# Optimization experiments

Hardware: AMD Instinct MI355X
Metric: run time of the kernel (lower is better)

The kernel has to match this reference:

```python
import jax, jax.numpy as jnp
import numpy as np

THRESH = 0.7
MIN_KEPT = 100000
IGNORE_LABEL = -100.0
LOG_CLAMP = -100.0  # torch binary_cross_entropy clamps log terms at -100

SHAPE = (32, 1, 1024, 1024)

def setup_inputs() -> dict:
    key = jax.random.key(0)
    k1, k2, k3 = jax.random.split(key, 3)
    eps = 1e-6
    predict = jax.random.uniform(k1, SHAPE, dtype=jnp.float32, minval=eps, maxval=1.0 - eps)
    target = jax.random.uniform(k2, SHAPE, dtype=jnp.float32)
    weight = jax.random.uniform(k3, SHAPE, dtype=jnp.float32)
    return {"predict": predict, "target": target, "weight": weight}

def reference(predict, target, weight):
    p = predict.reshape(-1)
    t = target.reshape(-1)
    w = weight.reshape(-1)

    mask = t != IGNORE_LABEL            # valid pixels
    n_valid = jnp.sum(mask)

    # k-th smallest valid probability -> OHEM threshold
    # (push ignored entries to +inf so they sort to the end)
    sort_p = jnp.sort(jnp.where(mask, p, jnp.inf))
    k = jnp.minimum(MIN_KEPT, n_valid - 1)
    min_threshold = sort_p[k]
    threshold = jnp.maximum(min_threshold, THRESH)

    # weighted BCE per element (torch semantics: clamp log at -100)
    logp = jnp.clip(jnp.log(p), LOG_CLAMP)
    log1mp = jnp.clip(jnp.log1p(-p), LOG_CLAMP)
    loss = -w * (t * logp + (1.0 - t) * log1mp)

    # selecting sorted losses where sort_prob < threshold == selecting
    # valid elements with p < threshold (sorting is a permutation)
    sel = mask & (p < threshold)
    total = jnp.sum(jnp.where(sel, loss, 0.0))
    count = jnp.sum(sel).astype(loss.dtype)
    return total / count  # reduction='elementwise_mean'
```

## Files before the change

kernel.cpp:

```cpp
#include <hip/hip_runtime.h>


#define OHEM_THRESH 0.7f
#define OHEM_MIN_KEPT 100000ULL
#define OHEM_IGNORE -100.0f
#define OHEM_LOG_CLAMP -100.0f

#define OHEM_BLOCKS 2048
#define OHEM_TPB 256

__device__ __forceinline__ void ohem_elem(float pp, float tt, float ww,
                                          float& lsum, unsigned int& lcnt,
                                          unsigned int& lval) {
    bool valid = (tt != OHEM_IGNORE);
    bool sel = valid && (pp < OHEM_THRESH);
    float logp = fmaxf(__logf(pp), OHEM_LOG_CLAMP);
    float log1mp = fmaxf(__logf(1.0f - pp), OHEM_LOG_CLAMP);
    float loss = -ww * (tt * logp + (1.0f - tt) * log1mp);
    lval += valid ? 1u : 0u;
    if (sel) {
        lsum += loss;
        lcnt += 1u;
    }
}

__global__ __launch_bounds__(OHEM_TPB, 4) void ohem_reduce(
    const float4* __restrict__ p4, const float4* __restrict__ t4,
    const float4* __restrict__ w4, float* __restrict__ psum,
    unsigned int* __restrict__ pcnt, unsigned int* __restrict__ pval,
    size_t n4, int NB, size_t G) {
    const int tid = threadIdx.x;
    const size_t g = (size_t)blockIdx.x * OHEM_TPB + tid;

    float lsum0 = 0.0f, lsum1 = 0.0f;
    unsigned int lcnt = 0, lval = 0;

    float4 pa0, pa1, ta0, ta1, wa0, wa1;
    float4 pb0, pb1, tb0, tb1, wb0, wb1;

#define LOADA(k)                                        \
    {                                                   \
        size_t i0 = (size_t)(k) * 2 * G + g;            \
        pa0 = p4[i0]; pa1 = p4[i0 + G];                 \
        ta0 = t4[i0]; ta1 = t4[i0 + G];                 \
        wa0 = w4[i0]; wa1 = w4[i0 + G];                 \
    }
#define LOADB(k)                                        \
    {                                                   \
        size_t i0 = (size_t)(k) * 2 * G + g;            \
        pb0 = p4[i0]; pb1 = p4[i0 + G];                 \
        tb0 = t4[i0]; tb1 = t4[i0 + G];                 \
        wb0 = w4[i0]; wb1 = w4[i0 + G];                 \
    }
#define COMP4(pv, tv, wv, ls)                           \
    {                                                   \
        ohem_elem(pv.x, tv.x, wv.x, ls, lcnt, lval);    \
        ohem_elem(pv.y, tv.y, wv.y, ls, lcnt, lval);    \
        ohem_elem(pv.z, tv.z, wv.z, ls, lcnt, lval);    \
        ohem_elem(pv.w, tv.w, wv.w, ls, lcnt, lval);    \
    }

    if (NB > 0) {
        LOADA(0);
        int k = 0;
        while (k + 2 <= NB) {
            LOADB(k + 1);
            __builtin_amdgcn_sched_barrier(0);
            COMP4(pa0, ta0, wa0, lsum0);
            COMP4(pa1, ta1, wa1, lsum1);
            if (k + 2 < NB) LOADA(k + 2);
            __builtin_amdgcn_sched_barrier(0);
            COMP4(pb0, tb0, wb0, lsum0);
            COMP4(pb1, tb1, wb1, lsum1);
            k += 2;
        }
        if (k < NB) {
            COMP4(pa0, ta0, wa0, lsum0);
            COMP4(pa1, ta1, wa1, lsum1);
        }
    }
    for (size_t i = (size_t)NB * 2 * G + g; i < n4; i += G) {
        float4 pv = p4[i];
        float4 tv = t4[i];
        float4 wv = w4[i];
        COMP4(pv, tv, wv, lsum0);
    }

    float lsum = lsum0 + lsum1;
#pragma unroll
    for (int off = 32; off > 0; off >>= 1) {
        lsum += __shfl_down(lsum, off, 64);
        lcnt += __shfl_down(lcnt, off, 64);
        lval += __shfl_down(lval, off, 64);
    }
    __shared__ float s_sum[4];
    __shared__ unsigned int s_cnt[4], s_val[4];
    const int wave = tid >> 6, lane = tid & 63;
    if (lane == 0) {
        s_sum[wave] = lsum;
        s_cnt[wave] = lcnt;
        s_val[wave] = lval;
    }
    __syncthreads();
    if (tid == 0) {
        psum[blockIdx.x] = s_sum[0] + s_sum[1] + s_sum[2] + s_sum[3];
        pcnt[blockIdx.x] = s_cnt[0] + s_cnt[1] + s_cnt[2] + s_cnt[3];
        pval[blockIdx.x] = s_val[0] + s_val[1] + s_val[2] + s_val[3];
    }
}

__global__ __launch_bounds__(256) void ohem_finalize(
    const float* __restrict__ p, const float* __restrict__ t,
    const float* __restrict__ w, const float* __restrict__ psum,
    const unsigned int* __restrict__ pcnt,
    const unsigned int* __restrict__ pval, int nblocks, int tail_start, int n,
    float* __restrict__ out) {
    const int tid = threadIdx.x;
    double dsum = 0.0;
    unsigned long long cnt = 0, val = 0;
    for (int i = tid; i < nblocks; i += 256) {
        dsum += (double)psum[i];
        cnt += pcnt[i];
        val += pval[i];
    }
    for (int i = tail_start + tid; i < n; i += 256) {
        float lsum = 0.0f;
        unsigned int lcnt = 0, lval = 0;
        ohem_elem(p[i], t[i], w[i], lsum, lcnt, lval);
        dsum += (double)lsum;
        cnt += lcnt;
        val += lval;
    }
#pragma unroll
    for (int off = 32; off > 0; off >>= 1) {
        dsum += __shfl_down(dsum, off, 64);
        cnt += __shfl_down(cnt, off, 64);
        val += __shfl_down(val, off, 64);
    }
    __shared__ double s_sum[4];
    __shared__ unsigned long long s_cnt[4], s_val[4];
    const int wave = tid >> 6, lane = tid & 63;
    if (lane == 0) {
        s_sum[wave] = dsum;
        s_cnt[wave] = cnt;
        s_val[wave] = val;
    }
    __syncthreads();
    if (tid == 0) {
        double fsum = s_sum[0] + s_sum[1] + s_sum[2] + s_sum[3];
        unsigned long long fcnt = s_cnt[0] + s_cnt[1] + s_cnt[2] + s_cnt[3];
        unsigned long long fval = s_val[0] + s_val[1] + s_val[2] + s_val[3];
        if (fval == 0) {
            out[0] = __builtin_nanf("");
            return;
        }
        unsigned long long k =
            (OHEM_MIN_KEPT < fval - 1) ? OHEM_MIN_KEPT : fval - 1;
        out[0] = (fcnt > k) ? (float)(fsum / (double)fcnt) : __builtin_nanf("");
    }
}

extern "C" void kernel_launch(void* const* d_in, const int* in_sizes, int n_in,
                              void* d_out, int out_size, void* d_ws,
                              size_t ws_size, hipStream_t stream) {
    const float* predict = (const float*)d_in[0];
    const float* target = (const float*)d_in[1];
    const float* weight = (const float*)d_in[2];
    float* out = (float*)d_out;
    const int n = in_sizes[0];
    const size_t n4 = (size_t)(n >> 2);
    const size_t G = (size_t)OHEM_BLOCKS * OHEM_TPB;
    const int NB = (int)(n4 / (2 * G));

    float* psum = (float*)d_ws;
    unsigned int* pcnt = (unsigned int*)(psum + OHEM_BLOCKS);
    unsigned int* pval = pcnt + OHEM_BLOCKS;

    hipLaunchKernelGGL(ohem_reduce, dim3(OHEM_BLOCKS), dim3(OHEM_TPB), 0,
                       stream, (const float4*)predict, (const float4*)target,
                       (const float4*)weight, psum, pcnt, pval, n4, NB, G);
    hipLaunchKernelGGL(ohem_finalize, dim3(1), dim3(256), 0, stream, predict,
                       target, weight, psum, pcnt, pval, OHEM_BLOCKS,
                       (int)(n4 << 2), n, out);
}
```

Before: 357.7 us.

## Replace double-buffered loads with 4-slot rotating inline-asm load pipeline

Replaces the two-stage A/B double buffer with a four-deep rotating pipeline built from inline-asm global_load_dwordx4 and explicit s_waitcnt vmcnt counters. Each slot is consumed and immediately refilled, so about nine loads stay in flight per thread while one group is computed. The goal is more memory-level parallelism on a bandwidth-bound streaming reduction. In exchange it raises register pressure, and the hand-written waitcnt accounting is fragile against compiler-inserted memory ops.

```diff
diff --git a/kernel.cpp b/kernel.cpp
--- a/kernel.cpp
+++ b/kernel.cpp
@@ -8,6 +8,9 @@
 
 #define OHEM_BLOCKS 2048
 #define OHEM_TPB 256
+#define OHEM_D 4
+
+typedef float f32x4 __attribute__((ext_vector_type(4)));
 
 __device__ __forceinline__ void ohem_elem(float pp, float tt, float ww,
                                           float& lsum, unsigned int& lcnt,
@@ -24,65 +27,78 @@
     }
 }
 
+#define COMP4(pv, tv, wv, ls)                                 \
+    {                                                         \
+        ohem_elem(pv[0], tv[0], wv[0], ls, lcnt, lval);       \
+        ohem_elem(pv[1], tv[1], wv[1], ls, lcnt, lval);       \
+        ohem_elem(pv[2], tv[2], wv[2], ls, lcnt, lval);       \
+        ohem_elem(pv[3], tv[3], wv[3], ls, lcnt, lval);       \
+    }
+
+#define GLOADX4(dst, ptr)                                                  \
+    asm volatile("global_load_dwordx4 %0, %1, off" : "=&v"(dst) : "v"(ptr))
+
+#define WAITCNT_SB(n)                                   \
+    do {                                                \
+        asm volatile("s_waitcnt vmcnt(" #n ")");        \
+        __builtin_amdgcn_sched_barrier(0);              \
+    } while (0)
+
 __global__ __launch_bounds__(OHEM_TPB, 4) void ohem_reduce(
-    const float4* __restrict__ p4, const float4* __restrict__ t4,
-    const float4* __restrict__ w4, float* __restrict__ psum,
+    const f32x4* __restrict__ p4, const f32x4* __restrict__ t4,
+    const f32x4* __restrict__ w4, float* __restrict__ psum,
     unsigned int* __restrict__ pcnt, unsigned int* __restrict__ pval,
-    size_t n4, int NB, size_t G) {
+    size_t n4, int NR, size_t G) {
     const int tid = threadIdx.x;
     const size_t g = (size_t)blockIdx.x * OHEM_TPB + tid;
 
     float lsum0 = 0.0f, lsum1 = 0.0f;
     unsigned int lcnt = 0, lval = 0;
 
-    float4 pa0, pa1, ta0, ta1, wa0, wa1;
-    float4 pb0, pb1, tb0, tb1, wb0, wb1;
-
-#define LOADA(k)                                        \
-    {                                                   \
-        size_t i0 = (size_t)(k) * 2 * G + g;            \
-        pa0 = p4[i0]; pa1 = p4[i0 + G];                 \
-        ta0 = t4[i0]; ta1 = t4[i0 + G];                 \
-        wa0 = w4[i0]; wa1 = w4[i0 + G];                 \
-    }
-#define LOADB(k)                                        \
-    {                                                   \
-        size_t i0 = (size_t)(k) * 2 * G + g;            \
-        pb0 = p4[i0]; pb1 = p4[i0 + G];                 \
-        tb0 = t4[i0]; tb1 = t4[i0 + G];                 \
-        wb0 = w4[i0]; wb1 = w4[i0 + G];                 \
-    }
-#define COMP4(pv, tv, wv, ls)                           \
-    {                                                   \
-        ohem_elem(pv.x, tv.x, wv.x, ls, lcnt, lval);    \
-        ohem_elem(pv.y, tv.y, wv.y, ls, lcnt, lval);    \
-        ohem_elem(pv.z, tv.z, wv.z, ls, lcnt, lval);    \
-        ohem_elem(pv.w, tv.w, wv.w, ls, lcnt, lval);    \
-    }
-
-    if (NB > 0) {
-        LOADA(0);
-        int k = 0;
-        while (k + 2 <= NB) {
-            LOADB(k + 1);
-            __builtin_amdgcn_sched_barrier(0);
-            COMP4(pa0, ta0, wa0, lsum0);
-            COMP4(pa1, ta1, wa1, lsum1);
-            if (k + 2 < NB) LOADA(k + 2);
-            __builtin_amdgcn_sched_barrier(0);
-            COMP4(pb0, tb0, wb0, lsum0);
-            COMP4(pb1, tb1, wb1, lsum1);
-            k += 2;
+    f32x4 P0, T0, W0, P1, T1, W1, P2, T2, W2, P3, T3, W3;
+
+    if (NR > 0) {
+        const f32x4* pp = p4 + g;
+        const f32x4* tp = t4 + g;
+        const f32x4* wp = w4 + g;
+        const size_t S = G;
+
+        GLOADX4(P0, pp);         GLOADX4(T0, tp);         GLOADX4(W0, wp);
+        GLOADX4(P1, pp + S);     GLOADX4(T1, tp + S);     GLOADX4(W1, wp + S);
+        GLOADX4(P2, pp + 2 * S); GLOADX4(T2, tp + 2 * S); GLOADX4(W2, wp + 2 * S);
+        GLOADX4(P3, pp + 3 * S); GLOADX4(T3, tp + 3 * S); GLOADX4(W3, wp + 3 * S);
+        pp += 4 * S; tp += 4 * S; wp += 4 * S;
+
+        for (int r = 0; r < NR - 1; ++r) {
+            WAITCNT_SB(9);
+            COMP4(P0, T0, W0, lsum0);
+            GLOADX4(P0, pp);         GLOADX4(T0, tp);         GLOADX4(W0, wp);
+            WAITCNT_SB(9);
+            COMP4(P1, T1, W1, lsum1);
+            GLOADX4(P1, pp + S);     GLOADX4(T1, tp + S);     GLOADX4(W1, wp + S);
+            WAITCNT_SB(9);
+            COMP4(P2, T2, W2, lsum0);
+            GLOADX4(P2, pp + 2 * S); GLOADX4(T2, tp + 2 * S); GLOADX4(W2, wp + 2 * S);
+            WAITCNT_SB(9);
+            COMP4(P3, T3, W3, lsum1);
+            GLOADX4(P3, pp + 3 * S); GLOADX4(T3, tp + 3 * S); GLOADX4(W3, wp + 3 * S);
+            pp += 4 * S; tp += 4 * S; wp += 4 * S;
         }
-        if (k < NB) {
-            COMP4(pa0, ta0, wa0, lsum0);
-            COMP4(pa1, ta1, wa1, lsum1);
-        }
-    }
-    for (size_t i = (size_t)NB * 2 * G + g; i < n4; i += G) {
-        float4 pv = p4[i];
-        float4 tv = t4[i];
-        float4 wv = w4[i];
+
+        WAITCNT_SB(9);
+        COMP4(P0, T0, W0, lsum0);
+        WAITCNT_SB(6);
+        COMP4(P1, T1, W1, lsum1);
+        WAITCNT_SB(3);
+        COMP4(P2, T2, W2, lsum0);
+        WAITCNT_SB(0);
+        COMP4(P3, T3, W3, lsum1);
+    }
+
+    for (size_t i = (size_t)NR * OHEM_D * G + g; i < n4; i += G) {
+        f32x4 pv = p4[i];
+        f32x4 tv = t4[i];
+        f32x4 wv = w4[i];
         COMP4(pv, tv, wv, lsum0);
     }
 
@@ -170,15 +186,15 @@
     const int n = in_sizes[0];
     const size_t n4 = (size_t)(n >> 2);
     const size_t G = (size_t)OHEM_BLOCKS * OHEM_TPB;
-    const int NB = (int)(n4 / (2 * G));
+    const int NR = (int)((n4 / G) / OHEM_D);
 
     float* psum = (float*)d_ws;
     unsigned int* pcnt = (unsigned int*)(psum + OHEM_BLOCKS);
     unsigned int* pval = pcnt + OHEM_BLOCKS;
 
     hipLaunchKernelGGL(ohem_reduce, dim3(OHEM_BLOCKS), dim3(OHEM_TPB), 0,
-                       stream, (const float4*)predict, (const float4*)target,
-                       (const float4*)weight, psum, pcnt, pval, n4, NB, G);
+                       stream, (const f32x4*)predict, (const f32x4*)target,
+                       (const f32x4*)weight, psum, pcnt, pval, n4, NR, G);
     hipLaunchKernelGGL(ohem_finalize, dim3(1), dim3(256), 0, stream, predict,
                        target, weight, psum, pcnt, pval, OHEM_BLOCKS,
                        (int)(n4 << 2), n, out);
```

Measured after the change: 359.3 us. No clear change (+0.4%).
